# Kernel tuning notes

Measured on AMD Instinct MI355X. Metric: run time of the kernel, lower is better.

## Reference

```python
import jax, jax.numpy as jnp
import numpy as np

# ---- fixed problem dimensions ----
B, S, T = 64, 200, 32          # batch of sequences, trees per seq, nodes per tree
V, E, C = 50000, 128, 128      # vocab, embedding_dim, encode_dim
H, OUT = 100, 104              # GRU hidden, output_dim
N = B * S * T                  # total nodes
D_MAX = 5                      # max depth of a 32-node complete binary tree


def setup_inputs() -> dict:
    key = jax.random.key(0)
    ks = jax.random.split(key, 16)
    # --- tree structure: every tree is a complete binary tree with T nodes ---
    local_parent = np.array([0] + [(i - 1) // 2 for i in range(1, T)], dtype=np.int64)
    local_depth = np.array([int(np.floor(np.log2(i + 1))) for i in range(T)], dtype=np.int64)
    num_trees = B * S
    offsets = np.arange(num_trees, dtype=np.int64) * T
    node_parent = (offsets[:, None] + local_parent[None, :]).reshape(-1)
    node_depth = np.tile(local_depth, num_trees)
    node_tree = np.repeat(np.arange(num_trees, dtype=np.int64), T)
    node_tokens = jax.random.randint(ks[0], (N,), 0, V, dtype=jnp.int64)
    sc = 0.05
    inp = {
        "node_tokens": node_tokens,
        "node_parent": jnp.asarray(node_parent),
        "node_tree": jnp.asarray(node_tree),
        "node_depth": jnp.asarray(node_depth),
        "emb": jax.random.normal(ks[1], (V, E), jnp.float32) * sc,
        "w_lin": jax.random.normal(ks[2], (C, E), jnp.float32) * sc,
        "b_lin": jnp.zeros((C,), jnp.float32),
        "w_ih_f": jax.random.normal(ks[3], (3 * H, C), jnp.float32) * sc,
        "w_hh_f": jax.random.normal(ks[4], (3 * H, H), jnp.float32) * sc,
        "b_ih_f": jnp.zeros((3 * H,), jnp.float32),
        "b_hh_f": jnp.zeros((3 * H,), jnp.float32),
        "w_ih_b": jax.random.normal(ks[5], (3 * H, C), jnp.float32) * sc,
        "w_hh_b": jax.random.normal(ks[6], (3 * H, H), jnp.float32) * sc,
        "b_ih_b": jnp.zeros((3 * H,), jnp.float32),
        "b_hh_b": jnp.zeros((3 * H,), jnp.float32),
        "fc_w": jax.random.normal(ks[7], (OUT, 2 * H), jnp.float32) * sc,
        "fc_b": jnp.zeros((OUT,), jnp.float32),
    }
    return inp


def _gru(x_sbc, w_ih, w_hh, b_ih, b_hh):
    """Torch-convention GRU over leading time axis. x_sbc: [S, B, C] -> [S, B, H]."""
    h0 = jnp.zeros((x_sbc.shape[1], w_hh.shape[1]), x_sbc.dtype)

    def step(h, xt):
        gx = xt @ w_ih.T + b_ih
        gh = h @ w_hh.T + b_hh
        xr, xz, xn = jnp.split(gx, 3, axis=-1)
        hr, hz, hn = jnp.split(gh, 3, axis=-1)
        r = jax.nn.sigmoid(xr + hr)
        z = jax.nn.sigmoid(xz + hz)
        n = jnp.tanh(xn + r * hn)
        h_new = (1.0 - z) * n + z * h
        return h_new, h_new

    _, hs = jax.lax.scan(step, h0, x_sbc)
    return hs


def reference(node_tokens, node_parent, node_tree, node_depth,
              emb, w_lin, b_lin,
              w_ih_f, w_hh_f, b_ih_f, b_hh_f,
              w_ih_b, w_hh_b, b_ih_b, b_hh_b,
              fc_w, fc_b):
    # per-node contribution: W * emb(token) + b   (recursion base of hidden_state)
    c = emb[node_tokens] @ w_lin.T + b_lin               # [N, C]
    # level-batched bottom-up scatter-add: h(node) = c(node) + sum(h(children))
    h = c
    for d in range(D_MAX, 0, -1):
        mask = (node_depth == d)[:, None]
        h = h.at[node_parent].add(jnp.where(mask, h, 0.0))
    # per-tree max pool over all node hidden states (TreeEncoder output)
    tree_vec = jax.ops.segment_max(h, node_tree, num_segments=B * S)  # [B*S, C]
    x = tree_vec.reshape(B, S, C)
    # bidirectional GRU (batch_first in torch; scan over time here)
    x_t = jnp.transpose(x, (1, 0, 2))                    # [S, B, C]
    fwd = _gru(x_t, w_ih_f, w_hh_f, b_ih_f, b_hh_f)      # [S, B, H]
    bwd = _gru(x_t[::-1], w_ih_b, w_hh_b, b_ih_b, b_hh_b)[::-1]
    gru_out = jnp.concatenate([fwd, bwd], axis=-1)       # [S, B, 2H]
    pool = gru_out.max(axis=0)                           # [B, 2H] (max over time)
    return pool @ fc_w.T + fc_b                          # [B, OUT]
```

## Files before the change

### kernel.cpp

```cpp
#include <hip/hip_runtime.h>
#include <hip/hip_bf16.h>
#include <math.h>

#define BB 64
#define SS 200
#define TT 32
#define EE 128
#define CC 128
#define HH 100
#define G3 300
#define OUTD 104
#define NTREE (BB*SS)

typedef __attribute__((ext_vector_type(8))) short short8;
typedef __attribute__((ext_vector_type(4))) float f32x4;
typedef _Float16 f16x8 __attribute__((ext_vector_type(8)));

__device__ inline unsigned short f2bf_rne(float f) {
    union { float f; unsigned u; } x; x.f = f;
    unsigned r = (x.u + 0x7FFFu + ((x.u >> 16) & 1u)) >> 16;
    return (unsigned short)r;
}
__device__ inline float bf2f(unsigned short h) {
    union { unsigned u; float f; } x; x.u = ((unsigned)h) << 16;
    return x.f;
}
__device__ inline float fast_sigmoid(float x) {
    return __builtin_amdgcn_rcpf(1.f + __builtin_amdgcn_exp2f(-1.4426950408889634f * x));
}
__device__ inline float fast_tanh(float x) {
    return 1.f - 2.f * __builtin_amdgcn_rcpf(1.f + __builtin_amdgcn_exp2f(2.8853900817779268f * x));
}

#define BAR() asm volatile("s_waitcnt lgkmcnt(0)\n\ts_barrier" ::: "memory")

#define K1_TPI 2
#define AROWS (K1_TPI*TT)
#define LDA 136
#define LDC 132

__global__ __launch_bounds__(256) void k1_mfma(const int* __restrict__ tok,
                                               const float* __restrict__ emb,
                                               const float* __restrict__ w_lin,
                                               const float* __restrict__ b_lin,
                                               float* __restrict__ tree_vec) {
    __shared__ __align__(16) unsigned short A_sh[AROWS * LDA];
    __shared__ __align__(16) float C_sh[AROWS * LDC];
    __shared__ int tok_sh[AROWS];

    const int tid  = threadIdx.x;
    const int wave = tid >> 6;
    const int lane = tid & 63;
    const int r = lane & 15;
    const int q = lane >> 4;

    short8 bfrag[2][4];
    float  bias[2];
#pragma unroll
    for (int nt = 0; nt < 2; ++nt) {
        const int n = wave * 32 + nt * 16 + r;
        bias[nt] = b_lin[n];
#pragma unroll
        for (int kt = 0; kt < 4; ++kt) {
            const float* src = w_lin + (long)n * EE + kt * 32 + q * 8;
            float4 a = ((const float4*)src)[0];
            float4 b = ((const float4*)src)[1];
            short8 f;
            f[0] = (short)f2bf_rne(a.x); f[1] = (short)f2bf_rne(a.y);
            f[2] = (short)f2bf_rne(a.z); f[3] = (short)f2bf_rne(a.w);
            f[4] = (short)f2bf_rne(b.x); f[5] = (short)f2bf_rne(b.y);
            f[6] = (short)f2bf_rne(b.z); f[7] = (short)f2bf_rne(b.w);
            bfrag[nt][kt] = f;
        }
    }

    const int tree0 = blockIdx.x * K1_TPI;
    if (tid < AROWS) tok_sh[tid] = tok[tree0 * TT + tid];
    __syncthreads();

#pragma unroll
    for (int i = 0; i < 8; ++i) {
        const int idx = tid + i * 256;
        const int row = idx >> 5;
        const int p   = idx & 31;
        const float4 e = ((const float4*)(emb + (long)tok_sh[row] * EE))[p];
        unsigned short* dst = &A_sh[row * LDA + p * 4];
        dst[0] = f2bf_rne(e.x); dst[1] = f2bf_rne(e.y);
        dst[2] = f2bf_rne(e.z); dst[3] = f2bf_rne(e.w);
    }
    __syncthreads();

    f32x4 acc[4][2];
#pragma unroll
    for (int mt = 0; mt < 4; ++mt)
#pragma unroll
        for (int nt = 0; nt < 2; ++nt) acc[mt][nt] = (f32x4)(0.f);

#pragma unroll
    for (int mt = 0; mt < 4; ++mt) {
        const int m = mt * 16 + r;
        short8 afrag[4];
#pragma unroll
        for (int kt = 0; kt < 4; ++kt)
            afrag[kt] = *(const short8*)&A_sh[m * LDA + kt * 32 + q * 8];
#pragma unroll
        for (int nt = 0; nt < 2; ++nt)
#pragma unroll
            for (int kt = 0; kt < 4; ++kt)
                acc[mt][nt] = __builtin_amdgcn_mfma_f32_16x16x32_bf16(
                    afrag[kt], bfrag[nt][kt], acc[mt][nt], 0, 0, 0);
    }

#pragma unroll
    for (int mt = 0; mt < 4; ++mt)
#pragma unroll
        for (int nt = 0; nt < 2; ++nt) {
            const int col = wave * 32 + nt * 16 + r;
#pragma unroll
            for (int reg = 0; reg < 4; ++reg) {
                const int row = mt * 16 + q * 4 + reg;
                C_sh[row * LDC + col] = acc[mt][nt][reg] + bias[nt];
            }
        }
    __syncthreads();

    {
        const int t = tid >> 7;
        const int j = tid & 127;
        const float* base = &C_sh[(t * TT) * LDC + j];
        float v[TT];
#pragma unroll
        for (int n = 0; n < TT; ++n) v[n] = base[n * LDC];
        float m = -1e30f;
#pragma unroll
        for (int n = TT - 1; n >= 1; --n) {
            m = fmaxf(m, v[n]);
            v[(n - 1) >> 1] += v[n];
        }
        m = fmaxf(m, v[0]);
        tree_vec[(long)(tree0 + t) * CC + j] = m;
    }
}

#define K2_NPAD 320
__global__ __launch_bounds__(256) void k2_mfma(const float* __restrict__ tree_vec,
                                               const float* __restrict__ w_ih_f,
                                               const float* __restrict__ b_ih_f,
                                               const float* __restrict__ w_ih_b,
                                               const float* __restrict__ b_ih_b,
                                               float* __restrict__ gx) {
    __shared__ __align__(16) unsigned short Ahi[32 * LDA];
    __shared__ __align__(16) unsigned short Alo[32 * LDA];
    __shared__ __align__(16) unsigned short Bhi[64 * LDA];
    __shared__ __align__(16) unsigned short Blo[64 * LDA];

    const int tid  = threadIdx.x;
    const int wave = tid >> 6;
    const int lane = tid & 63;
    const int r = lane & 15;
    const int q = lane >> 4;

    const int nb = blockIdx.x % 10;
    const int mb = blockIdx.x / 10;
    const int m0 = mb * 32;
    const int n0 = nb * 64;

#pragma unroll
    for (int i = 0; i < 4; ++i) {
        const int idx = tid + i * 256;
        const int row = idx >> 5;
        const int p   = idx & 31;
        const float4 v = ((const float4*)(tree_vec + (long)(m0 + row) * CC))[p];
        unsigned short* dh = &Ahi[row * LDA + p * 4];
        unsigned short* dl = &Alo[row * LDA + p * 4];
        float e[4] = {v.x, v.y, v.z, v.w};
#pragma unroll
        for (int c = 0; c < 4; ++c) {
            unsigned short h = f2bf_rne(e[c]);
            dh[c] = h;
            dl[c] = f2bf_rne(e[c] - bf2f(h));
        }
    }
#pragma unroll
    for (int i = 0; i < 8; ++i) {
        const int idx = tid + i * 256;
        const int row = idx >> 5;
        const int p   = idx & 31;
        const int n   = n0 + row;
        const int dir = (n >= K2_NPAD) ? 1 : 0;
        const int j   = n - dir * K2_NPAD;
        const int jj  = (j < G3) ? j : 0;
        const float* w = dir ? w_ih_b : w_ih_f;
        const float4 v = ((const float4*)(w + (long)jj * EE))[p];
        unsigned short* dh = &Bhi[row * LDA + p * 4];
        unsigned short* dl = &Blo[row * LDA + p * 4];
        float e[4] = {v.x, v.y, v.z, v.w};
#pragma unroll
        for (int c = 0; c < 4; ++c) {
            unsigned short h = f2bf_rne(e[c]);
            dh[c] = h;
            dl[c] = f2bf_rne(e[c] - bf2f(h));
        }
    }
    __syncthreads();

    const int nloc = wave * 16 + r;
    short8 bh[4], bl[4];
#pragma unroll
    for (int kt = 0; kt < 4; ++kt) {
        bh[kt] = *(const short8*)&Bhi[nloc * LDA + kt * 32 + q * 8];
        bl[kt] = *(const short8*)&Blo[nloc * LDA + kt * 32 + q * 8];
    }

    f32x4 acc[2];
    acc[0] = (f32x4)(0.f); acc[1] = (f32x4)(0.f);
#pragma unroll
    for (int mt = 0; mt < 2; ++mt) {
        const int m = mt * 16 + r;
#pragma unroll
        for (int kt = 0; kt < 4; ++kt) {
            short8 ah = *(const short8*)&Ahi[m * LDA + kt * 32 + q * 8];
            short8 al = *(const short8*)&Alo[m * LDA + kt * 32 + q * 8];
            acc[mt] = __builtin_amdgcn_mfma_f32_16x16x32_bf16(ah, bh[kt], acc[mt], 0, 0, 0);
            acc[mt] = __builtin_amdgcn_mfma_f32_16x16x32_bf16(ah, bl[kt], acc[mt], 0, 0, 0);
            acc[mt] = __builtin_amdgcn_mfma_f32_16x16x32_bf16(al, bh[kt], acc[mt], 0, 0, 0);
        }
    }

    const int ng  = n0 + wave * 16 + r;
    const int dir = (ng >= K2_NPAD) ? 1 : 0;
    const int j   = ng - dir * K2_NPAD;
    const bool valid = (j < G3);
    const float bias = valid ? (dir ? b_ih_b[j] : b_ih_f[j]) : 0.f;
    float* gxd = gx + (long)dir * NTREE * G3;
    if (valid) {
#pragma unroll
        for (int mt = 0; mt < 2; ++mt)
#pragma unroll
            for (int reg = 0; reg < 4; ++reg) {
                const int m = m0 + mt * 16 + q * 4 + reg;
                gxd[(long)m * G3 + j] = acc[mt][reg] + bias;
            }
    }
}

__global__ __launch_bounds__(256, 1) void k3_gru(const float* __restrict__ gx,
                                                 const float* __restrict__ w_hh_f,
                                                 const float* __restrict__ b_hh_f,
                                                 const float* __restrict__ w_hh_b,
                                                 const float* __restrict__ b_hh_b,
                                                 float* __restrict__ pool) {
    const int bid = blockIdx.x;
    const int dir = bid & 1;
    const int b = bid >> 1;
    const float* w_hh = dir ? w_hh_b : w_hh_f;
    const float* b_hh = dir ? b_hh_b : b_hh_f;

    __shared__ __align__(16) _Float16 h_sh[2][128];
    __shared__ float g_sh[4][80];

    const int tid  = threadIdx.x;
    const int wave = tid >> 6;
    const int lane = tid & 63;
    const int r = lane & 15;
    const int q = lane >> 4;

    f16x8 bf[5][4];
#pragma unroll
    for (int i = 0; i < 5; ++i) {
        const int l = i * 16 + r;
        const int gate = l / 25;
        const int ch   = l - gate * 25;
        const bool nv  = (l < 75);
        const int row  = gate * HH + wave * 25 + ch;
#pragma unroll
        for (int kt = 0; kt < 4; ++kt) {
            f16x8 f;
#pragma unroll
            for (int e = 0; e < 8; ++e) {
                const int k = kt * 32 + q * 8 + e;
                f[e] = (_Float16)((nv && k < HH) ? w_hh[row * HH + k] : 0.f);
            }
            bf[i][kt] = f;
        }
    }

    const int m = lane;
    const int c = wave * 25 + m;
    const bool act = (m < 25);
    float br = 0.f, bz = 0.f, bn = 0.f;
    if (act) { br = b_hh[c]; bz = b_hh[HH + c]; bn = b_hh[2 * HH + c]; }

    if (tid < 128) { h_sh[0][tid] = (_Float16)0.f; h_sh[1][tid] = (_Float16)0.f; }

    const float* gxd = gx + (long)dir * NTREE * G3;
    const int sstep = dir ? -1 : 1;
    int s = dir ? (SS - 1) : 0;
    float xr = 0.f, xz = 0.f, xn = 0.f;
    if (act) {
        const float* row0 = gxd + ((long)b * SS + s) * G3;
        xr = row0[c]; xz = row0[HH + c]; xn = row0[2 * HH + c];
    }
    float hj = 0.f, hmax = -1e30f;
    __syncthreads();

    for (int t = 0; t < SS; ++t) {
        const int p = t & 1;
        const int s_n = s + sstep;
        float xrn = 0.f, xzn = 0.f, xnn = 0.f;
        if (act && t < SS - 1) {
            const float* row0 = gxd + ((long)b * SS + s_n) * G3;
            xrn = row0[c]; xzn = row0[HH + c]; xnn = row0[2 * HH + c];
        }

        f16x8 a[4];
#pragma unroll
        for (int kt = 0; kt < 4; ++kt)
            a[kt] = *(const f16x8*)&h_sh[p][kt * 32 + q * 8];
        f32x4 acc[5];
#pragma unroll
        for (int i = 0; i < 5; ++i) {
            acc[i] = (f32x4)(0.f);
#pragma unroll
            for (int kt = 0; kt < 4; ++kt)
                acc[i] = __builtin_amdgcn_mfma_f32_16x16x32_f16(a[kt], bf[i][kt], acc[i], 0, 0, 0);
        }
        if (q == 0) {
#pragma unroll
            for (int i = 0; i < 5; ++i)
                g_sh[wave][i * 16 + r] = acc[i][0];
        }
        if (act) {
            const float ghr = g_sh[wave][m];
            const float ghz = g_sh[wave][25 + m];
            const float ghn = g_sh[wave][50 + m];
            const float rg = fast_sigmoid(xr + ghr + br);
            const float zg = fast_sigmoid(xz + ghz + bz);
            const float ng = fast_tanh(xn + rg * (ghn + bn));
            hj = (1.f - zg) * ng + zg * hj;
            hmax = fmaxf(hmax, hj);
            h_sh[1 - p][c] = (_Float16)hj;
            xr = xrn; xz = xzn; xn = xnn;
        }
        BAR();
        s = s_n;
    }
    if (act) pool[(long)b * (2 * HH) + dir * HH + c] = hmax;
}

__global__ __launch_bounds__(256) void k4_fc(const float* __restrict__ pool,
                                             const float* __restrict__ fc_w,
                                             const float* __restrict__ fc_b,
                                             float* __restrict__ out) {
    const int b = blockIdx.x;
    __shared__ __align__(16) float p_sh[2 * HH];
    const int t = threadIdx.x;
    if (t < 2 * HH) p_sh[t] = pool[(long)b * (2 * HH) + t];
    __syncthreads();
    if (t < OUTD) {
        const float4* wr4 = (const float4*)(fc_w + (long)t * (2 * HH));
        const float4* p4 = (const float4*)p_sh;
        float a0 = 0.f, a1 = 0.f;
#pragma unroll
        for (int k = 0; k < 50; k += 2) {
            float4 w0 = wr4[k],   p0 = p4[k];
            float4 w1 = wr4[k+1], p1 = p4[k+1];
            a0 += w0.x*p0.x + w0.y*p0.y + w0.z*p0.z + w0.w*p0.w;
            a1 += w1.x*p1.x + w1.y*p1.y + w1.z*p1.z + w1.w*p1.w;
        }
        out[(long)b * OUTD + t] = fc_b[t] + a0 + a1;
    }
}

extern "C" void kernel_launch(void* const* d_in, const int* in_sizes, int n_in,
                              void* d_out, int out_size, void* d_ws, size_t ws_size,
                              hipStream_t stream) {
    const int*   tok    = (const int*)d_in[0];
    const float* emb    = (const float*)d_in[4];
    const float* w_lin  = (const float*)d_in[5];
    const float* b_lin  = (const float*)d_in[6];
    const float* w_ih_f = (const float*)d_in[7];
    const float* w_hh_f = (const float*)d_in[8];
    const float* b_ih_f = (const float*)d_in[9];
    const float* b_hh_f = (const float*)d_in[10];
    const float* w_ih_b = (const float*)d_in[11];
    const float* w_hh_b = (const float*)d_in[12];
    const float* b_ih_b = (const float*)d_in[13];
    const float* b_hh_b = (const float*)d_in[14];
    const float* fc_w   = (const float*)d_in[15];
    const float* fc_b   = (const float*)d_in[16];

    float* ws       = (float*)d_ws;
    float* tree_vec = ws;
    float* gx       = tree_vec + (long)NTREE * CC;
    float* pool     = gx + (long)2 * NTREE * G3;
    float* out      = (float*)d_out;

    k1_mfma<<<NTREE / K1_TPI, 256, 0, stream>>>(tok, emb, w_lin, b_lin, tree_vec);
    k2_mfma<<<(NTREE / 32) * 10, 256, 0, stream>>>(tree_vec, w_ih_f, b_ih_f, w_ih_b, b_ih_b, gx);
    k3_gru <<<2 * BB, 256, 0, stream>>>(gx, w_hh_f, b_hh_f, w_hh_b, b_hh_b, pool);
    k4_fc  <<<BB, 256, 0, stream>>>(pool, fc_w, fc_b, out);
}
```

Before: 276.5 us.

## Switch GEMMs to fp16 MFMA with pre-swizzled weights and fp16 tree vectors

Adds a prep kernel that converts w_lin and the GRU input weights to fp16 in MFMA fragment order, so k1 and k2 load fragments directly instead of converting per block. k1 now uses f16 MFMA and writes tree vectors in fp16. k2 drops the bf16 hi/lo split-precision trick and does a single f16 MFMA per tile, while also halving its input traffic. The trade is lower accuracy in the input projection and an extra kernel launch.

```diff
diff --git a/kernel.cpp b/kernel.cpp
--- a/kernel.cpp
+++ b/kernel.cpp
@@ -12,19 +12,9 @@
 #define OUTD 104
 #define NTREE (BB*SS)
 
-typedef __attribute__((ext_vector_type(8))) short short8;
 typedef __attribute__((ext_vector_type(4))) float f32x4;
 typedef _Float16 f16x8 __attribute__((ext_vector_type(8)));
 
-__device__ inline unsigned short f2bf_rne(float f) {
-    union { float f; unsigned u; } x; x.f = f;
-    unsigned r = (x.u + 0x7FFFu + ((x.u >> 16) & 1u)) >> 16;
-    return (unsigned short)r;
-}
-__device__ inline float bf2f(unsigned short h) {
-    union { unsigned u; float f; } x; x.u = ((unsigned)h) << 16;
-    return x.f;
-}
 __device__ inline float fast_sigmoid(float x) {
     return __builtin_amdgcn_rcpf(1.f + __builtin_amdgcn_exp2f(-1.4426950408889634f * x));
 }
@@ -34,44 +24,75 @@
 
 #define BAR() asm volatile("s_waitcnt lgkmcnt(0)\n\ts_barrier" ::: "memory")
 
-#define K1_TPI 2
-#define AROWS (K1_TPI*TT)
-#define LDA 136
-#define LDC 132
-
-__global__ __launch_bounds__(256) void k1_mfma(const int* __restrict__ tok,
-                                               const float* __restrict__ emb,
-                                               const float* __restrict__ w_lin,
-                                               const float* __restrict__ b_lin,
-                                               float* __restrict__ tree_vec) {
-    __shared__ __align__(16) unsigned short A_sh[AROWS * LDA];
-    __shared__ __align__(16) float C_sh[AROWS * LDC];
-    __shared__ int tok_sh[AROWS];
-
+
+__global__ __launch_bounds__(256) void k0_prep(const float* __restrict__ w_lin,
+                                               const float* __restrict__ w_ih_f,
+                                               const float* __restrict__ w_ih_b,
+                                               _Float16* __restrict__ wl,
+                                               _Float16* __restrict__ k2b) {
     const int tid  = threadIdx.x;
     const int wave = tid >> 6;
     const int lane = tid & 63;
     const int r = lane & 15;
     const int q = lane >> 4;
-
-    short8 bfrag[2][4];
-    float  bias[2];
+    if (blockIdx.x == 0) {
+#pragma unroll
+        for (int nt = 0; nt < 2; ++nt)
+#pragma unroll
+            for (int kt = 0; kt < 4; ++kt) {
+                const int n = wave * 32 + nt * 16 + r;
+                const float* src = w_lin + (long)n * EE + kt * 32 + q * 8;
+                f16x8 f;
+#pragma unroll
+                for (int e = 0; e < 8; ++e) f[e] = (_Float16)src[e];
+                *(f16x8*)&wl[(size_t)((((wave * 2 + nt) * 4 + kt) * 64) + lane) * 8] = f;
+            }
+    } else {
+        const int nb = blockIdx.x - 1;
+        const int n = nb * 64 + wave * 16 + r;
+        const int dir = (n >= 320) ? 1 : 0;
+        const int j = n - dir * 320;
+        const int jj = (j < G3) ? j : 0;
+        const float* w = dir ? w_ih_b : w_ih_f;
+#pragma unroll
+        for (int kt = 0; kt < 4; ++kt) {
+            const float* src = w + (long)jj * EE + kt * 32 + q * 8;
+            f16x8 f;
+#pragma unroll
+            for (int e = 0; e < 8; ++e) f[e] = (_Float16)src[e];
+            *(f16x8*)&k2b[(size_t)((((nb * 4 + wave) * 4 + kt) * 64) + lane) * 8] = f;
+        }
+    }
+}
+
+#define K1_TPI 2
+#define AROWS (K1_TPI*TT)
+#define LDA 136
+#define LDC 132
+
+__global__ __launch_bounds__(256) void k1_mfma(const int* __restrict__ tok,
+                                               const float* __restrict__ emb,
+                                               const _Float16* __restrict__ wl,
+                                               const float* __restrict__ b_lin,
+                                               _Float16* __restrict__ thi) {
+    __shared__ __align__(16) _Float16 A_sh[AROWS * LDA];
+    __shared__ __align__(16) float C_sh[AROWS * LDC];
+    __shared__ int tok_sh[AROWS];
+
+    const int tid  = threadIdx.x;
+    const int wave = tid >> 6;
+    const int lane = tid & 63;
+    const int r = lane & 15;
+    const int q = lane >> 4;
+
+    f16x8 bfrag[2][4];
+    float bias[2];
 #pragma unroll
     for (int nt = 0; nt < 2; ++nt) {
-        const int n = wave * 32 + nt * 16 + r;
-        bias[nt] = b_lin[n];
-#pragma unroll
-        for (int kt = 0; kt < 4; ++kt) {
-            const float* src = w_lin + (long)n * EE + kt * 32 + q * 8;
-            float4 a = ((const float4*)src)[0];
-            float4 b = ((const float4*)src)[1];
-            short8 f;
-            f[0] = (short)f2bf_rne(a.x); f[1] = (short)f2bf_rne(a.y);
-            f[2] = (short)f2bf_rne(a.z); f[3] = (short)f2bf_rne(a.w);
-            f[4] = (short)f2bf_rne(b.x); f[5] = (short)f2bf_rne(b.y);
-            f[6] = (short)f2bf_rne(b.z); f[7] = (short)f2bf_rne(b.w);
-            bfrag[nt][kt] = f;
-        }
+        bias[nt] = b_lin[wave * 32 + nt * 16 + r];
+#pragma unroll
+        for (int kt = 0; kt < 4; ++kt)
+            bfrag[nt][kt] = *(const f16x8*)&wl[(size_t)((((wave * 2 + nt) * 4 + kt) * 64) + lane) * 8];
     }
 
     const int tree0 = blockIdx.x * K1_TPI;
@@ -84,9 +105,9 @@
         const int row = idx >> 5;
         const int p   = idx & 31;
         const float4 e = ((const float4*)(emb + (long)tok_sh[row] * EE))[p];
-        unsigned short* dst = &A_sh[row * LDA + p * 4];
-        dst[0] = f2bf_rne(e.x); dst[1] = f2bf_rne(e.y);
-        dst[2] = f2bf_rne(e.z); dst[3] = f2bf_rne(e.w);
+        _Float16* dst = &A_sh[row * LDA + p * 4];
+        dst[0] = (_Float16)e.x; dst[1] = (_Float16)e.y;
+        dst[2] = (_Float16)e.z; dst[3] = (_Float16)e.w;
     }
     __syncthreads();
 
@@ -99,15 +120,15 @@
 #pragma unroll
     for (int mt = 0; mt < 4; ++mt) {
         const int m = mt * 16 + r;
-        short8 afrag[4];
+        f16x8 afrag[4];
 #pragma unroll
         for (int kt = 0; kt < 4; ++kt)
-            afrag[kt] = *(const short8*)&A_sh[m * LDA + kt * 32 + q * 8];
+            afrag[kt] = *(const f16x8*)&A_sh[m * LDA + kt * 32 + q * 8];
 #pragma unroll
         for (int nt = 0; nt < 2; ++nt)
 #pragma unroll
             for (int kt = 0; kt < 4; ++kt)
-                acc[mt][nt] = __builtin_amdgcn_mfma_f32_16x16x32_bf16(
+                acc[mt][nt] = __builtin_amdgcn_mfma_f32_16x16x32_f16(
                     afrag[kt], bfrag[nt][kt], acc[mt][nt], 0, 0, 0);
     }
 
@@ -131,28 +152,23 @@
         float v[TT];
 #pragma unroll
         for (int n = 0; n < TT; ++n) v[n] = base[n * LDC];
-        float m = -1e30f;
+        float mx = -1e30f;
 #pragma unroll
         for (int n = TT - 1; n >= 1; --n) {
-            m = fmaxf(m, v[n]);
+            mx = fmaxf(mx, v[n]);
             v[(n - 1) >> 1] += v[n];
         }
-        m = fmaxf(m, v[0]);
-        tree_vec[(long)(tree0 + t) * CC + j] = m;
-    }
-}
-
-#define K2_NPAD 320
-__global__ __launch_bounds__(256) void k2_mfma(const float* __restrict__ tree_vec,
-                                               const float* __restrict__ w_ih_f,
+        mx = fmaxf(mx, v[0]);
+        thi[(size_t)(tree0 + t) * CC + j] = (_Float16)mx;
+    }
+}
+
+__global__ __launch_bounds__(256) void k2_mfma(const _Float16* __restrict__ thi,
+                                               const _Float16* __restrict__ k2b,
                                                const float* __restrict__ b_ih_f,
-                                               const float* __restrict__ w_ih_b,
                                                const float* __restrict__ b_ih_b,
                                                float* __restrict__ gx) {
-    __shared__ __align__(16) unsigned short Ahi[32 * LDA];
-    __shared__ __align__(16) unsigned short Alo[32 * LDA];
-    __shared__ __align__(16) unsigned short Bhi[64 * LDA];
-    __shared__ __align__(16) unsigned short Blo[64 * LDA];
+    __shared__ __align__(16) _Float16 Ah[32 * LDA];
 
     const int tid  = threadIdx.x;
     const int wave = tid >> 6;
@@ -166,51 +182,18 @@
     const int n0 = nb * 64;
 
 #pragma unroll
-    for (int i = 0; i < 4; ++i) {
+    for (int i = 0; i < 2; ++i) {
         const int idx = tid + i * 256;
-        const int row = idx >> 5;
-        const int p   = idx & 31;
-        const float4 v = ((const float4*)(tree_vec + (long)(m0 + row) * CC))[p];
-        unsigned short* dh = &Ahi[row * LDA + p * 4];
-        unsigned short* dl = &Alo[row * LDA + p * 4];
-        float e[4] = {v.x, v.y, v.z, v.w};
-#pragma unroll
-        for (int c = 0; c < 4; ++c) {
-            unsigned short h = f2bf_rne(e[c]);
-            dh[c] = h;
-            dl[c] = f2bf_rne(e[c] - bf2f(h));
-        }
-    }
-#pragma unroll
-    for (int i = 0; i < 8; ++i) {
-        const int idx = tid + i * 256;
-        const int row = idx >> 5;
-        const int p   = idx & 31;
-        const int n   = n0 + row;
-        const int dir = (n >= K2_NPAD) ? 1 : 0;
-        const int j   = n - dir * K2_NPAD;
-        const int jj  = (j < G3) ? j : 0;
-        const float* w = dir ? w_ih_b : w_ih_f;
-        const float4 v = ((const float4*)(w + (long)jj * EE))[p];
-        unsigned short* dh = &Bhi[row * LDA + p * 4];
-        unsigned short* dl = &Blo[row * LDA + p * 4];
-        float e[4] = {v.x, v.y, v.z, v.w};
-#pragma unroll
-        for (int c = 0; c < 4; ++c) {
-            unsigned short h = f2bf_rne(e[c]);
-            dh[c] = h;
-            dl[c] = f2bf_rne(e[c] - bf2f(h));
-        }
-    }
-    __syncthreads();
-
-    const int nloc = wave * 16 + r;
-    short8 bh[4], bl[4];
-#pragma unroll
-    for (int kt = 0; kt < 4; ++kt) {
-        bh[kt] = *(const short8*)&Bhi[nloc * LDA + kt * 32 + q * 8];
-        bl[kt] = *(const short8*)&Blo[nloc * LDA + kt * 32 + q * 8];
-    }
+        const int row = idx >> 4;
+        const int p   = idx & 15;
+        f16x8 v = *(const f16x8*)&thi[(size_t)(m0 + row) * CC + p * 8];
+        *(f16x8*)&Ah[row * LDA + p * 8] = v;
+    }
+    f16x8 bh[4];
+#pragma unroll
+    for (int kt = 0; kt < 4; ++kt)
+        bh[kt] = *(const f16x8*)&k2b[(size_t)((((nb * 4 + wave) * 4 + kt) * 64) + lane) * 8];
+    __syncthreads();
 
     f32x4 acc[2];
     acc[0] = (f32x4)(0.f); acc[1] = (f32x4)(0.f);
@@ -219,17 +202,14 @@
         const int m = mt * 16 + r;
 #pragma unroll
         for (int kt = 0; kt < 4; ++kt) {
-            short8 ah = *(const short8*)&Ahi[m * LDA + kt * 32 + q * 8];
-            short8 al = *(const short8*)&Alo[m * LDA + kt * 32 + q * 8];
-            acc[mt] = __builtin_amdgcn_mfma_f32_16x16x32_bf16(ah, bh[kt], acc[mt], 0, 0, 0);
-            acc[mt] = __builtin_amdgcn_mfma_f32_16x16x32_bf16(ah, bl[kt], acc[mt], 0, 0, 0);
-            acc[mt] = __builtin_amdgcn_mfma_f32_16x16x32_bf16(al, bh[kt], acc[mt], 0, 0, 0);
+            f16x8 a = *(const f16x8*)&Ah[m * LDA + kt * 32 + q * 8];
+            acc[mt] = __builtin_amdgcn_mfma_f32_16x16x32_f16(a, bh[kt], acc[mt], 0, 0, 0);
         }
     }
 
     const int ng  = n0 + wave * 16 + r;
-    const int dir = (ng >= K2_NPAD) ? 1 : 0;
-    const int j   = ng - dir * K2_NPAD;
+    const int dir = (ng >= 320) ? 1 : 0;
+    const int j   = ng - dir * 320;
     const bool valid = (j < G3);
     const float bias = valid ? (dir ? b_ih_b[j] : b_ih_f[j]) : 0.f;
     float* gxd = gx + (long)dir * NTREE * G3;
@@ -390,14 +370,17 @@
     const float* fc_w   = (const float*)d_in[15];
     const float* fc_b   = (const float*)d_in[16];
 
-    float* ws       = (float*)d_ws;
-    float* tree_vec = ws;
-    float* gx       = tree_vec + (long)NTREE * CC;
-    float* pool     = gx + (long)2 * NTREE * G3;
-    float* out      = (float*)d_out;
-
-    k1_mfma<<<NTREE / K1_TPI, 256, 0, stream>>>(tok, emb, w_lin, b_lin, tree_vec);
-    k2_mfma<<<(NTREE / 32) * 10, 256, 0, stream>>>(tree_vec, w_ih_f, b_ih_f, w_ih_b, b_ih_b, gx);
+    char* wsb = (char*)d_ws;
+    _Float16* wl   = (_Float16*)(wsb);
+    _Float16* k2b  = (_Float16*)(wsb + 32768);
+    _Float16* thi  = (_Float16*)(wsb + 196608);
+    float*    gx   = (float*)(wsb + 3473408);
+    float*    pool = (float*)(wsb);
+    float*    out  = (float*)d_out;
+
+    k0_prep<<<11, 256, 0, stream>>>(w_lin, w_ih_f, w_ih_b, wl, k2b);
+    k1_mfma<<<NTREE / K1_TPI, 256, 0, stream>>>(tok, emb, wl, b_lin, thi);
+    k2_mfma<<<(NTREE / 32) * 10, 256, 0, stream>>>(thi, k2b, b_ih_f, b_ih_b, gx);
     k3_gru <<<2 * BB, 256, 0, stream>>>(gx, w_hh_f, b_hh_f, w_hh_b, b_hh_b, pool);
     k4_fc  <<<BB, 256, 0, stream>>>(pool, fc_w, fc_b, out);
 }
```

Result: faster. 245.7 us (-11.1%).
